# Performance work log

Measured on AMD Instinct MI355X. Metric: run time of the kernel, lower is better.

The kernel has to match this reference:

```python
import jax, jax.numpy as jnp
import numpy as np

N_NODES = 50000
N_EDGES = 800000
DIM = 128
NUM_LAYERS = 4


def setup_inputs() -> dict:
    key = jax.random.key(0)
    ks = jax.random.split(key, 7)
    x = jax.random.normal(ks[0], (N_NODES, DIM), dtype=jnp.float32)
    edge_index = jax.random.randint(ks[1], (2, N_EDGES), 0, N_NODES, dtype=jnp.int64)
    batch = jnp.zeros((N_NODES,), dtype=jnp.int64)
    scale = 1.0 / np.sqrt(DIM)
    W1 = jax.random.normal(ks[2], (NUM_LAYERS, DIM, DIM), dtype=jnp.float32) * scale
    b1 = jax.random.normal(ks[3], (NUM_LAYERS, DIM), dtype=jnp.float32) * scale
    W2 = jax.random.normal(ks[4], (NUM_LAYERS, DIM, DIM), dtype=jnp.float32) * scale
    b2 = jax.random.normal(ks[5], (NUM_LAYERS, DIM), dtype=jnp.float32) * scale
    return {"x": x, "edge_index": edge_index, "batch": batch,
            "W1": W1, "b1": b1, "W2": W2, "b2": b2}


def reference(x, edge_index, batch, W1, b1, W2, b2):
    # Stacked GINConv (eps=0): h = MLP(x + sum_{j->i} x_j)
    src, dst = edge_index[0], edge_index[1]
    for l in range(NUM_LAYERS):
        agg = x + jax.ops.segment_sum(x[src], dst, num_segments=N_NODES)
        h = jax.nn.relu(agg @ W1[l] + b1[l])
        x = h @ W2[l] + b2[l]
    return x
```

## Files before the change

kernel.cpp:

```cpp
#include <hip/hip_runtime.h>
#include <hip/hip_bf16.h>
#include <cstdint>

#define N_NODES 50000
#define N_EDGES 800000
#define DIM     128
#define NLAYERS 4

#define SCAN_BLK 256
#define NB ((N_NODES + SCAN_BLK - 1) / SCAN_BLK)


__global__ __launch_bounds__(256) void zero_kernel(int* __restrict__ p, int n) {
    int i = blockIdx.x * blockDim.x + threadIdx.x;
    if (i < n) p[i] = 0;
}

__global__ __launch_bounds__(256) void count_kernel(const int* __restrict__ key,
                                                    int* __restrict__ cnt) {
    int e = blockIdx.x * blockDim.x + threadIdx.x;
    if (e < N_EDGES) atomicAdd(&cnt[key[e]], 1);
}

__global__ __launch_bounds__(SCAN_BLK) void scanA(const int* __restrict__ cnt,
                                                  int* __restrict__ off,
                                                  int* __restrict__ bsum) {
    __shared__ int s[SCAN_BLK];
    const int t = threadIdx.x;
    const int i = blockIdx.x * SCAN_BLK + t;
    int v = (i < N_NODES) ? cnt[i] : 0;
    s[t] = v;
    __syncthreads();
    for (int d = 1; d < SCAN_BLK; d <<= 1) {
        int add = (t >= d) ? s[t - d] : 0;
        __syncthreads();
        s[t] += add;
        __syncthreads();
    }
    if (i < N_NODES) off[i] = s[t] - v;
    if (t == SCAN_BLK - 1) bsum[blockIdx.x] = s[t];
}

__global__ __launch_bounds__(SCAN_BLK) void scanB(int* __restrict__ bsum) {
    __shared__ int s[SCAN_BLK];
    const int t = threadIdx.x;
    int v = (t < NB) ? bsum[t] : 0;
    s[t] = v;
    __syncthreads();
    for (int d = 1; d < SCAN_BLK; d <<= 1) {
        int add = (t >= d) ? s[t - d] : 0;
        __syncthreads();
        s[t] += add;
        __syncthreads();
    }
    if (t < NB) bsum[t] = s[t] - v;
}

__global__ __launch_bounds__(SCAN_BLK) void scanC(int* __restrict__ off,
                                                  const int* __restrict__ bsum,
                                                  int* __restrict__ cur) {
    const int i = blockIdx.x * SCAN_BLK + threadIdx.x;
    if (i < N_NODES) {
        int o = off[i] + bsum[blockIdx.x];
        off[i] = o;
        cur[i] = o;
    }
    if (i == 0) off[N_NODES] = N_EDGES;
}

__global__ __launch_bounds__(256) void scatter_kernel(const int* __restrict__ src,
                                                      const int* __restrict__ dst,
                                                      int* __restrict__ cur,
                                                      int* __restrict__ csr) {
    int e = blockIdx.x * blockDim.x + threadIdx.x;
    if (e < N_EDGES) {
        int d = dst[e];
        int pos = atomicAdd(&cur[d], 1);
        csr[pos] = src[e];
    }
}


static __device__ __forceinline__ float bf2f(unsigned short u) {
    unsigned v = (unsigned)u << 16;
    float f;
    __builtin_memcpy(&f, &v, 4);
    return f;
}
static __device__ __forceinline__ unsigned short f2bf(float f) {
    __hip_bfloat16 h = __float2bfloat16(f);
    unsigned short u;
    __builtin_memcpy(&u, &h, 2);
    return u;
}

__global__ __launch_bounds__(256) void conv_kernel(const float* __restrict__ x,
                                                   unsigned short* __restrict__ xh) {
    int i = blockIdx.x * blockDim.x + threadIdx.x;
    const int n4 = N_NODES * DIM / 4;
    if (i < n4) {
        float4 v = reinterpret_cast<const float4*>(x)[i];
        ushort4 h;
        h.x = f2bf(v.x); h.y = f2bf(v.y); h.z = f2bf(v.z); h.w = f2bf(v.w);
        reinterpret_cast<ushort4*>(xh)[i] = h;
    }
}


#define RT 32
#define LDW 132
#define MAXE 1024

__global__ __launch_bounds__(256) void gin_layer(
    const float* __restrict__ xin,
    const unsigned short* __restrict__ xh,
    const int* __restrict__ off,
    const int* __restrict__ csr,
    const float* __restrict__ W1, const float* __restrict__ b1,
    const float* __restrict__ W2, const float* __restrict__ b2,
    float* __restrict__ xout,
    unsigned short* __restrict__ xhout)
{
    __shared__ float sA[RT][LDW];
    __shared__ int   sIdx[MAXE];
    __shared__ int   sOff[RT + 1];
    const int tid  = threadIdx.x;
    const int base = blockIdx.x * RT;
    const int rtop = min(RT, N_NODES - base);

    if (tid <= rtop) sOff[tid] = off[base + tid];
    __syncthreads();

    const int e0 = sOff[0];
    const int nE = sOff[rtop] - e0;
    const bool staged = (nE <= MAXE);
    if (staged) {
        for (int i = tid; i < nE; i += 256) sIdx[i] = csr[e0 + i];
    }
    __syncthreads();

    {
        const int c = tid & 31;
        const int g = tid >> 5;
        const float4*  xin4 = reinterpret_cast<const float4*>(xin);
        const ushort4* xh4  = reinterpret_cast<const ushort4*>(xh);
        #pragma unroll
        for (int it = 0; it < 4; ++it) {
            const int rr = g + it * 8;
            if (rr < rtop) {
                const int node = base + rr;
                float4 a = xin4[node * 32 + c];
                const int k0 = sOff[rr] - e0, k1 = sOff[rr + 1] - e0;
                int k = k0;
                if (staged) {
                    for (; k + 8 <= k1; k += 8) {
                        int id[8];
                        #pragma unroll
                        for (int j = 0; j < 8; ++j) id[j] = sIdx[k + j];
                        ushort4 u0 = xh4[id[0] * 32 + c];
                        ushort4 u1 = xh4[id[1] * 32 + c];
                        ushort4 u2 = xh4[id[2] * 32 + c];
                        ushort4 u3 = xh4[id[3] * 32 + c];
                        ushort4 u4 = xh4[id[4] * 32 + c];
                        ushort4 u5 = xh4[id[5] * 32 + c];
                        ushort4 u6 = xh4[id[6] * 32 + c];
                        ushort4 u7 = xh4[id[7] * 32 + c];
                        a.x += ((bf2f(u0.x) + bf2f(u1.x)) + (bf2f(u2.x) + bf2f(u3.x))) +
                               ((bf2f(u4.x) + bf2f(u5.x)) + (bf2f(u6.x) + bf2f(u7.x)));
                        a.y += ((bf2f(u0.y) + bf2f(u1.y)) + (bf2f(u2.y) + bf2f(u3.y))) +
                               ((bf2f(u4.y) + bf2f(u5.y)) + (bf2f(u6.y) + bf2f(u7.y)));
                        a.z += ((bf2f(u0.z) + bf2f(u1.z)) + (bf2f(u2.z) + bf2f(u3.z))) +
                               ((bf2f(u4.z) + bf2f(u5.z)) + (bf2f(u6.z) + bf2f(u7.z)));
                        a.w += ((bf2f(u0.w) + bf2f(u1.w)) + (bf2f(u2.w) + bf2f(u3.w))) +
                               ((bf2f(u4.w) + bf2f(u5.w)) + (bf2f(u6.w) + bf2f(u7.w)));
                    }
                    for (; k < k1; ++k) {
                        ushort4 u = xh4[sIdx[k] * 32 + c];
                        a.x += bf2f(u.x); a.y += bf2f(u.y);
                        a.z += bf2f(u.z); a.w += bf2f(u.w);
                    }
                } else {
                    for (; k < k1; ++k) {
                        ushort4 u = xh4[csr[e0 + k] * 32 + c];
                        a.x += bf2f(u.x); a.y += bf2f(u.y);
                        a.z += bf2f(u.z); a.w += bf2f(u.w);
                    }
                }
                *reinterpret_cast<float4*>(&sA[rr][c * 4]) = a;
            }
        }
    }
    __syncthreads();

    const int tc = tid & 31;
    const int tr = tid >> 5;

    float acc[4][4] = {};
    {
        const float4* Wv = reinterpret_cast<const float4*>(W1);
        #pragma unroll 4
        for (int k4 = 0; k4 < DIM / 4; ++k4) {
            float4 w[4];
            #pragma unroll
            for (int j = 0; j < 4; ++j) w[j] = Wv[(k4 * 4 + j) * 32 + tc];
            #pragma unroll
            for (int i = 0; i < 4; ++i) {
                const float4 a = *reinterpret_cast<const float4*>(&sA[tr * 4 + i][k4 * 4]);
                acc[i][0] += a.x * w[0].x + a.y * w[1].x + a.z * w[2].x + a.w * w[3].x;
                acc[i][1] += a.x * w[0].y + a.y * w[1].y + a.z * w[2].y + a.w * w[3].y;
                acc[i][2] += a.x * w[0].z + a.y * w[1].z + a.z * w[2].z + a.w * w[3].z;
                acc[i][3] += a.x * w[0].w + a.y * w[1].w + a.z * w[2].w + a.w * w[3].w;
            }
        }
        const float4 b = reinterpret_cast<const float4*>(b1)[tc];
        #pragma unroll
        for (int i = 0; i < 4; ++i) {
            acc[i][0] = fmaxf(acc[i][0] + b.x, 0.f);
            acc[i][1] = fmaxf(acc[i][1] + b.y, 0.f);
            acc[i][2] = fmaxf(acc[i][2] + b.z, 0.f);
            acc[i][3] = fmaxf(acc[i][3] + b.w, 0.f);
        }
    }
    __syncthreads();

    #pragma unroll
    for (int i = 0; i < 4; ++i) {
        float4 h;
        h.x = acc[i][0]; h.y = acc[i][1]; h.z = acc[i][2]; h.w = acc[i][3];
        *reinterpret_cast<float4*>(&sA[tr * 4 + i][tc * 4]) = h;
    }
    __syncthreads();

    {
        float acc2[4][4] = {};
        const float4* Wv = reinterpret_cast<const float4*>(W2);
        #pragma unroll 4
        for (int k4 = 0; k4 < DIM / 4; ++k4) {
            float4 w[4];
            #pragma unroll
            for (int j = 0; j < 4; ++j) w[j] = Wv[(k4 * 4 + j) * 32 + tc];
            #pragma unroll
            for (int i = 0; i < 4; ++i) {
                const float4 a = *reinterpret_cast<const float4*>(&sA[tr * 4 + i][k4 * 4]);
                acc2[i][0] += a.x * w[0].x + a.y * w[1].x + a.z * w[2].x + a.w * w[3].x;
                acc2[i][1] += a.x * w[0].y + a.y * w[1].y + a.z * w[2].y + a.w * w[3].y;
                acc2[i][2] += a.x * w[0].z + a.y * w[1].z + a.z * w[2].z + a.w * w[3].z;
                acc2[i][3] += a.x * w[0].w + a.y * w[1].w + a.z * w[2].w + a.w * w[3].w;
            }
        }
        const float4 b = reinterpret_cast<const float4*>(b2)[tc];
        #pragma unroll
        for (int i = 0; i < 4; ++i) {
            const int node = base + tr * 4 + i;
            if (node < N_NODES) {
                float4 o;
                o.x = acc2[i][0] + b.x;
                o.y = acc2[i][1] + b.y;
                o.z = acc2[i][2] + b.z;
                o.w = acc2[i][3] + b.w;
                reinterpret_cast<float4*>(xout + node * DIM)[tc] = o;
                ushort4 h;
                h.x = f2bf(o.x); h.y = f2bf(o.y); h.z = f2bf(o.z); h.w = f2bf(o.w);
                reinterpret_cast<ushort4*>(xhout + node * DIM)[tc] = h;
            }
        }
    }
}


extern "C" void kernel_launch(void* const* d_in, const int* in_sizes, int n_in,
                              void* d_out, int out_size, void* d_ws, size_t ws_size,
                              hipStream_t stream) {
    const float* x  = (const float*)d_in[0];
    const int*   ei = (const int*)d_in[1];
    const float* W1 = (const float*)d_in[3];
    const float* b1 = (const float*)d_in[4];
    const float* W2 = (const float*)d_in[5];
    const float* b2 = (const float*)d_in[6];
    float* out = (float*)d_out;

    const int* src = ei;
    const int* dst = ei + N_EDGES;

    float*          bufA = (float*)d_ws;
    unsigned short* xhA  = (unsigned short*)(bufA + (size_t)N_NODES * DIM);
    unsigned short* xhB  = xhA + (size_t)N_NODES * DIM;
    int*   cnt  = (int*)(xhB + (size_t)N_NODES * DIM);
    int*   offs = cnt + N_NODES;
    int*   cur  = offs + N_NODES + 1;
    int*   bsum = cur + N_NODES;
    int*   csr  = bsum + 256;

    zero_kernel<<<NB, 256, 0, stream>>>(cnt, N_NODES);
    count_kernel<<<(N_EDGES + 255) / 256, 256, 0, stream>>>(dst, cnt);
    scanA<<<NB, SCAN_BLK, 0, stream>>>(cnt, offs, bsum);
    scanB<<<1, SCAN_BLK, 0, stream>>>(bsum);
    scanC<<<NB, SCAN_BLK, 0, stream>>>(offs, bsum, cur);
    scatter_kernel<<<(N_EDGES + 255) / 256, 256, 0, stream>>>(src, dst, cur, csr);

    conv_kernel<<<(N_NODES * DIM / 4 + 255) / 256, 256, 0, stream>>>(x, xhA);

    const int nblk = (N_NODES + RT - 1) / RT;
    gin_layer<<<nblk, 256, 0, stream>>>(x, xhA, offs, csr,
                                        W1 + 0 * DIM * DIM, b1 + 0 * DIM,
                                        W2 + 0 * DIM * DIM, b2 + 0 * DIM, bufA, xhB);
    gin_layer<<<nblk, 256, 0, stream>>>(bufA, xhB, offs, csr,
                                        W1 + 1 * DIM * DIM, b1 + 1 * DIM,
                                        W2 + 1 * DIM * DIM, b2 + 1 * DIM, out, xhA);
    gin_layer<<<nblk, 256, 0, stream>>>(out, xhA, offs, csr,
                                        W1 + 2 * DIM * DIM, b1 + 2 * DIM,
                                        W2 + 2 * DIM * DIM, b2 + 2 * DIM, bufA, xhB);
    gin_layer<<<nblk, 256, 0, stream>>>(bufA, xhB, offs, csr,
                                        W1 + 3 * DIM * DIM, b1 + 3 * DIM,
                                        W2 + 3 * DIM * DIM, b2 + 3 * DIM, out, xhA);
}
```

Baseline: 677.2 us.

## Split fused GIN layer into separate aggregation and MLP kernels

The fused gather+MLP kernel is split into an aggregation kernel (one warp-row per node, indices broadcast by shuffle, up to 32 gathers in flight) and an MLP kernel that reads the aggregated rows from a global buffer. The goal is to decouple the latency-bound gather from the compute-bound MLP so each can use its own occupancy and gather more memory-level parallelism. The cost is an extra float32 round trip of the full node feature matrix and twice as many launches per layer. The output buffer is reused as scratch for the aggregate.

```diff
diff --git a/kernel.cpp b/kernel.cpp
--- a/kernel.cpp
+++ b/kernel.cpp
@@ -107,86 +107,77 @@
 }
 
 
-#define RT 32
-#define LDW 132
-#define MAXE 1024
-
-__global__ __launch_bounds__(256) void gin_layer(
+__global__ __launch_bounds__(256) void agg_kernel(
     const float* __restrict__ xin,
     const unsigned short* __restrict__ xh,
     const int* __restrict__ off,
     const int* __restrict__ csr,
+    float* __restrict__ agg)
+{
+    const int tid  = threadIdx.x;
+    const int c    = tid & 31;
+    const int node = blockIdx.x * 8 + (tid >> 5);
+    if (node >= N_NODES) return;
+
+    const float4*  xin4 = reinterpret_cast<const float4*>(xin);
+    const ushort4* xh4  = reinterpret_cast<const ushort4*>(xh);
+
+    const int k0 = off[node], k1 = off[node + 1];
+    float4 a = xin4[node * 32 + c];
+
+    for (int kb = k0; kb < k1; kb += 32) {
+        const int m = min(32, k1 - kb);
+        int idxv = (c < m) ? csr[kb + c] : 0;
+        ushort4 v[16], v2[16];
+        #pragma unroll
+        for (int j = 0; j < 16; ++j) {
+            int id = __shfl(idxv, j, 32);
+            if (j < m) v[j] = xh4[id * 32 + c];
+        }
+        #pragma unroll
+        for (int j = 0; j < 16; ++j) {
+            int id = __shfl(idxv, j + 16, 32);
+            if (j + 16 < m) v2[j] = xh4[id * 32 + c];
+        }
+        #pragma unroll
+        for (int j = 0; j < 16; ++j) {
+            if (j < m) {
+                a.x += bf2f(v[j].x); a.y += bf2f(v[j].y);
+                a.z += bf2f(v[j].z); a.w += bf2f(v[j].w);
+            }
+        }
+        #pragma unroll
+        for (int j = 0; j < 16; ++j) {
+            if (j + 16 < m) {
+                a.x += bf2f(v2[j].x); a.y += bf2f(v2[j].y);
+                a.z += bf2f(v2[j].z); a.w += bf2f(v2[j].w);
+            }
+        }
+    }
+    reinterpret_cast<float4*>(agg)[node * 32 + c] = a;
+}
+
+
+#define RT 32
+#define LDW 132
+
+__global__ __launch_bounds__(256) void mlp_kernel(
+    const float* __restrict__ agg,
     const float* __restrict__ W1, const float* __restrict__ b1,
     const float* __restrict__ W2, const float* __restrict__ b2,
     float* __restrict__ xout,
     unsigned short* __restrict__ xhout)
 {
     __shared__ float sA[RT][LDW];
-    __shared__ int   sIdx[MAXE];
-    __shared__ int   sOff[RT + 1];
     const int tid  = threadIdx.x;
     const int base = blockIdx.x * RT;
-    const int rtop = min(RT, N_NODES - base);
-
-    if (tid <= rtop) sOff[tid] = off[base + tid];
-    __syncthreads();
-
-    const int e0 = sOff[0];
-    const int nE = sOff[rtop] - e0;
-    const bool staged = (nE <= MAXE);
-    if (staged) {
-        for (int i = tid; i < nE; i += 256) sIdx[i] = csr[e0 + i];
-    }
-    __syncthreads();
 
     {
-        const int c = tid & 31;
-        const int g = tid >> 5;
-        const float4*  xin4 = reinterpret_cast<const float4*>(xin);
-        const ushort4* xh4  = reinterpret_cast<const ushort4*>(xh);
-        #pragma unroll
-        for (int it = 0; it < 4; ++it) {
-            const int rr = g + it * 8;
-            if (rr < rtop) {
-                const int node = base + rr;
-                float4 a = xin4[node * 32 + c];
-                const int k0 = sOff[rr] - e0, k1 = sOff[rr + 1] - e0;
-                int k = k0;
-                if (staged) {
-                    for (; k + 8 <= k1; k += 8) {
-                        int id[8];
-                        #pragma unroll
-                        for (int j = 0; j < 8; ++j) id[j] = sIdx[k + j];
-                        ushort4 u0 = xh4[id[0] * 32 + c];
-                        ushort4 u1 = xh4[id[1] * 32 + c];
-                        ushort4 u2 = xh4[id[2] * 32 + c];
-                        ushort4 u3 = xh4[id[3] * 32 + c];
-                        ushort4 u4 = xh4[id[4] * 32 + c];
-                        ushort4 u5 = xh4[id[5] * 32 + c];
-                        ushort4 u6 = xh4[id[6] * 32 + c];
-                        ushort4 u7 = xh4[id[7] * 32 + c];
-                        a.x += ((bf2f(u0.x) + bf2f(u1.x)) + (bf2f(u2.x) + bf2f(u3.x))) +
-                               ((bf2f(u4.x) + bf2f(u5.x)) + (bf2f(u6.x) + bf2f(u7.x)));
-                        a.y += ((bf2f(u0.y) + bf2f(u1.y)) + (bf2f(u2.y) + bf2f(u3.y))) +
-                               ((bf2f(u4.y) + bf2f(u5.y)) + (bf2f(u6.y) + bf2f(u7.y)));
-                        a.z += ((bf2f(u0.z) + bf2f(u1.z)) + (bf2f(u2.z) + bf2f(u3.z))) +
-                               ((bf2f(u4.z) + bf2f(u5.z)) + (bf2f(u6.z) + bf2f(u7.z)));
-                        a.w += ((bf2f(u0.w) + bf2f(u1.w)) + (bf2f(u2.w) + bf2f(u3.w))) +
-                               ((bf2f(u4.w) + bf2f(u5.w)) + (bf2f(u6.w) + bf2f(u7.w)));
-                    }
-                    for (; k < k1; ++k) {
-                        ushort4 u = xh4[sIdx[k] * 32 + c];
-                        a.x += bf2f(u.x); a.y += bf2f(u.y);
-                        a.z += bf2f(u.z); a.w += bf2f(u.w);
-                    }
-                } else {
-                    for (; k < k1; ++k) {
-                        ushort4 u = xh4[csr[e0 + k] * 32 + c];
-                        a.x += bf2f(u.x); a.y += bf2f(u.y);
-                        a.z += bf2f(u.z); a.w += bf2f(u.w);
-                    }
-                }
-                *reinterpret_cast<float4*>(&sA[rr][c * 4]) = a;
+        const float4* agg4 = reinterpret_cast<const float4*>(agg);
+        for (int i = tid; i < RT * 32; i += 256) {
+            const int r = i >> 5, cc = i & 31;
+            if (base + r < N_NODES) {
+                *reinterpret_cast<float4*>(&sA[r][cc * 4]) = agg4[(base + r) * 32 + cc];
             }
         }
     }
@@ -290,6 +281,7 @@
     int*   cur  = offs + N_NODES + 1;
     int*   bsum = cur + N_NODES;
     int*   csr  = bsum + 256;
+    float* G    = out;
 
     zero_kernel<<<NB, 256, 0, stream>>>(cnt, N_NODES);
     count_kernel<<<(N_EDGES + 255) / 256, 256, 0, stream>>>(dst, cnt);
@@ -300,17 +292,19 @@
 
     conv_kernel<<<(N_NODES * DIM / 4 + 255) / 256, 256, 0, stream>>>(x, xhA);
 
-    const int nblk = (N_NODES + RT - 1) / RT;
-    gin_layer<<<nblk, 256, 0, stream>>>(x, xhA, offs, csr,
-                                        W1 + 0 * DIM * DIM, b1 + 0 * DIM,
-                                        W2 + 0 * DIM * DIM, b2 + 0 * DIM, bufA, xhB);
-    gin_layer<<<nblk, 256, 0, stream>>>(bufA, xhB, offs, csr,
-                                        W1 + 1 * DIM * DIM, b1 + 1 * DIM,
-                                        W2 + 1 * DIM * DIM, b2 + 1 * DIM, out, xhA);
-    gin_layer<<<nblk, 256, 0, stream>>>(out, xhA, offs, csr,
-                                        W1 + 2 * DIM * DIM, b1 + 2 * DIM,
-                                        W2 + 2 * DIM * DIM, b2 + 2 * DIM, bufA, xhB);
-    gin_layer<<<nblk, 256, 0, stream>>>(bufA, xhB, offs, csr,
-                                        W1 + 3 * DIM * DIM, b1 + 3 * DIM,
-                                        W2 + 3 * DIM * DIM, b2 + 3 * DIM, out, xhA);
-}
+    const int nblk_agg = (N_NODES + 7) / 8;
+    const int nblk_mlp = (N_NODES + RT - 1) / RT;
+
+    agg_kernel<<<nblk_agg, 256, 0, stream>>>(x, xhA, offs, csr, G);
+    mlp_kernel<<<nblk_mlp, 256, 0, stream>>>(G, W1 + 0 * DIM * DIM, b1 + 0 * DIM,
+                                             W2 + 0 * DIM * DIM, b2 + 0 * DIM, bufA, xhB);
+    agg_kernel<<<nblk_agg, 256, 0, stream>>>(bufA, xhB, offs, csr, G);
+    mlp_kernel<<<nblk_mlp, 256, 0, stream>>>(G, W1 + 1 * DIM * DIM, b1 + 1 * DIM,
+                                             W2 + 1 * DIM * DIM, b2 + 1 * DIM, bufA, xhA);
+    agg_kernel<<<nblk_agg, 256, 0, stream>>>(bufA, xhA, offs, csr, G);
+    mlp_kernel<<<nblk_mlp, 256, 0, stream>>>(G, W1 + 2 * DIM * DIM, b1 + 2 * DIM,
+                                             W2 + 2 * DIM * DIM, b2 + 2 * DIM, bufA, xhB);
+    agg_kernel<<<nblk_agg, 256, 0, stream>>>(bufA, xhB, offs, csr, G);
+    mlp_kernel<<<nblk_mlp, 256, 0, stream>>>(G, W1 + 3 * DIM * DIM, b1 + 3 * DIM,
+                                             W2 + 3 * DIM * DIM, b2 + 3 * DIM, out, xhA);
+}
```

After: 634.1 us. -6.4%, faster.
